# Performance work log

Hardware: AMD Instinct MI355X
Metric: run time of the kernel (lower is better)

The kernel has to match this reference:

```python
import jax, jax.numpy as jnp
import numpy as np

T = 20.0  # temperature
SCALE = 0.3

def reference(outputs1, outputs2, outputs3, outputs4, outputs5, outputs6, outputs7, outputs8, targets):
    # preds: [M=8, B, C] tempered softmaxes
    logits = jnp.stack([outputs1, outputs2, outputs3, outputs4,
                        outputs5, outputs6, outputs7, outputs8], axis=0)
    preds = jax.nn.softmax(logits / T, axis=-1)
    # center over class dim (Pearson correlation per sample per model)
    v = preds - jnp.mean(preds, axis=-1, keepdims=True)
    v = v / jnp.sqrt(jnp.sum(v * v, axis=-1, keepdims=True))  # unit-norm rows
    # Gram over model pairs: [B, M, M]
    G = jnp.einsum('mbc,nbc->bmn', v, v)
    M = G.shape[-1]
    # sum over upper triangle (j<k); diagonal entries are exactly 1 pre-normalization
    d = (jnp.sum(G, axis=(1, 2)) - jnp.trace(G, axis1=1, axis2=2)) * 0.5  # [B]
    loss = SCALE * d
    return jnp.mean(loss)

def setup_inputs() -> dict:
    key = jax.random.key(0)
    ks = jax.random.split(key, 9)
    B, C = 4096, 1000
    inp = {f'outputs{i+1}': jax.random.normal(ks[i], (B, C), dtype=jnp.float32)
           for i in range(8)}
    inp['targets'] = jax.random.randint(ks[8], (B,), 0, C, dtype=jnp.int64)
    return inp
```

## Files before the change

### kernel.cpp

```cpp
#include <hip/hip_runtime.h>
#include <math.h>


constexpr int NC    = 1000;
constexpr int NC4   = 250;
constexpr int NM    = 8;
constexpr int NPAIR = NM * (NM + 1) / 2;
constexpr float KEXP = 0.072134752044448169f;
constexpr float INVC = 1.0f / (float)NC;

__device__ __forceinline__ float waveSum(float v) {
#pragma unroll
    for (int o = 32; o > 0; o >>= 1) v += __shfl_xor(v, o, 64);
    return v;
}
__device__ __forceinline__ double waveSumD(double v) {
#pragma unroll
    for (int o = 32; o > 0; o >>= 1) v += __shfl_xor(v, o, 64);
    return v;
}
__device__ __forceinline__ constexpr int tidx(int m, int n) {
    return m * (2 * NM - m + 1) / 2 + (n - m);
}

__global__ __launch_bounds__(256, 2) void div8_main(
    const float* __restrict__ in0, const float* __restrict__ in1,
    const float* __restrict__ in2, const float* __restrict__ in3,
    const float* __restrict__ in4, const float* __restrict__ in5,
    const float* __restrict__ in6, const float* __restrict__ in7,
    float* __restrict__ part, int B)
{
    const int wid  = threadIdx.x >> 6;
    const int lane = threadIdx.x & 63;
    const int b    = blockIdx.x * 4 + wid;
    if (b >= B) return;
    const bool act3 = lane < (NC4 - 3 * 64);

    const float4* p[NM] = {
        reinterpret_cast<const float4*>(in0 + (size_t)b * NC),
        reinterpret_cast<const float4*>(in1 + (size_t)b * NC),
        reinterpret_cast<const float4*>(in2 + (size_t)b * NC),
        reinterpret_cast<const float4*>(in3 + (size_t)b * NC),
        reinterpret_cast<const float4*>(in4 + (size_t)b * NC),
        reinterpret_cast<const float4*>(in5 + (size_t)b * NC),
        reinterpret_cast<const float4*>(in6 + (size_t)b * NC),
        reinterpret_cast<const float4*>(in7 + (size_t)b * NC) };

    const int   idx[4] = { lane, lane + 64, lane + 128, act3 ? lane + 192 : NC4 - 1 };
    const float msk[4] = { 1.f, 1.f, 1.f, act3 ? 1.f : 0.f };

    float D[NPAIR];
    float t[NM];
#pragma unroll
    for (int k = 0; k < NPAIR; ++k) D[k] = 0.f;
#pragma unroll
    for (int m = 0; m < NM; ++m) t[m] = 0.f;

    float4 cur[NM], nxt[NM];
#pragma unroll
    for (int m = 0; m < NM; ++m) cur[m] = p[m][idx[0]];

#pragma unroll
    for (int j = 0; j < 4; ++j) {
        if (j < 3) {
#pragma unroll
            for (int m = 0; m < NM; ++m) nxt[m] = p[m][idx[j + 1]];
        }
        const float mj = msk[j];
#pragma unroll
        for (int m = 0; m < NM; ++m) {
            cur[m].x = (exp2f(cur[m].x * KEXP) - 1.f) * mj;
            cur[m].y = (exp2f(cur[m].y * KEXP) - 1.f) * mj;
            cur[m].z = (exp2f(cur[m].z * KEXP) - 1.f) * mj;
            cur[m].w = (exp2f(cur[m].w * KEXP) - 1.f) * mj;
        }
#pragma unroll
        for (int comp = 0; comp < 4; ++comp) {
            float us[NM];
#pragma unroll
            for (int m = 0; m < NM; ++m)
                us[m] = (comp == 0) ? cur[m].x : (comp == 1) ? cur[m].y
                      : (comp == 2) ? cur[m].z : cur[m].w;
#pragma unroll
            for (int m = 0; m < NM; ++m) {
                t[m] += us[m];
#pragma unroll
                for (int n = m; n < NM; ++n)
                    D[tidx(m, n)] = fmaf(us[m], us[n], D[tidx(m, n)]);
            }
        }
        if (j < 3) {
#pragma unroll
            for (int m = 0; m < NM; ++m) cur[m] = nxt[m];
        }
    }

#pragma unroll
    for (int k = 0; k < NPAIR; ++k) D[k] = waveSum(D[k]);
#pragma unroll
    for (int m = 0; m < NM; ++m) t[m] = waveSum(t[m]);

    float rm[NM];
#pragma unroll
    for (int m = 0; m < NM; ++m) {
        float q = fmaf(-t[m] * INVC, t[m], D[tidx(m, m)]);
        rm[m] = 1.0f / sqrtf(q);
    }
    double cr = 0.0;
#pragma unroll
    for (int m = 0; m < NM; ++m)
#pragma unroll
        for (int n = m + 1; n < NM; ++n) {
            float cov = fmaf(-t[m] * INVC, t[n], D[tidx(m, n)]);
            cr += (double)(cov * rm[m] * rm[n]);
        }
    if (lane == 0) part[b] = (float)(2.0 * cr);
}

__global__ __launch_bounds__(256) void div8_final(
    const float* __restrict__ part, float* __restrict__ out, int B)
{
    const int t = threadIdx.x;
    double acc = 0.0;
    for (int i = t; i < B; i += 256) acc += (double)part[i];
    acc = waveSumD(acc);
    __shared__ double redd[4];
    if ((t & 63) == 0) redd[t >> 6] = acc;
    __syncthreads();
    if (t == 0) {
        double tot = (redd[0] + redd[1]) + (redd[2] + redd[3]);
        out[0] = (float)(tot * (0.5 * 0.3 / (double)B));
    }
}

extern "C" void kernel_launch(void* const* d_in, const int* in_sizes, int n_in,
                              void* d_out, int out_size, void* d_ws, size_t ws_size,
                              hipStream_t stream)
{
    const float* a0 = (const float*)d_in[0];
    const float* a1 = (const float*)d_in[1];
    const float* a2 = (const float*)d_in[2];
    const float* a3 = (const float*)d_in[3];
    const float* a4 = (const float*)d_in[4];
    const float* a5 = (const float*)d_in[5];
    const float* a6 = (const float*)d_in[6];
    const float* a7 = (const float*)d_in[7];
    const int B = in_sizes[0] / NC;

    float* part = (float*)d_ws;

    const int grid = (B + 3) / 4;
    div8_main<<<grid, 256, 0, stream>>>(a0, a1, a2, a3, a4, a5, a6, a7, part, B);
    div8_final<<<1, 256, 0, stream>>>(part, (float*)d_out, B);
}
```

Before: 38.41 us.

## Split each row across two waves and combine partial Gram sums via LDS

Each sample row is now processed by two wavefronts, each loading two float4 chunks per model up front instead of four with a software-prefetch chain. Partial Gram and sum accumulators are reduced per wave, exchanged through shared memory with a block barrier, and the final correlation is computed from the combined values. The grid doubles and the launch-bounds occupancy hint is dropped. The aim is more memory-level parallelism and shorter per-wave serial work, at the cost of an extra reduction, a barrier and duplicated epilogue math.

```diff
diff --git a/kernel.cpp b/kernel.cpp
--- a/kernel.cpp
+++ b/kernel.cpp
@@ -6,6 +6,7 @@
 constexpr int NC4   = 250;
 constexpr int NM    = 8;
 constexpr int NPAIR = NM * (NM + 1) / 2;
+constexpr int NRED  = NPAIR + NM;
 constexpr float KEXP = 0.072134752044448169f;
 constexpr float INVC = 1.0f / (float)NC;
 
@@ -23,7 +24,7 @@
     return m * (2 * NM - m + 1) / 2 + (n - m);
 }
 
-__global__ __launch_bounds__(256, 2) void div8_main(
+__global__ __launch_bounds__(256) void div8_main(
     const float* __restrict__ in0, const float* __restrict__ in1,
     const float* __restrict__ in2, const float* __restrict__ in3,
     const float* __restrict__ in4, const float* __restrict__ in5,
@@ -32,11 +33,13 @@
 {
     const int wid  = threadIdx.x >> 6;
     const int lane = threadIdx.x & 63;
-    const int b    = blockIdx.x * 4 + wid;
-    if (b >= B) return;
-    const bool act3 = lane < (NC4 - 3 * 64);
+    const int half = wid & 1;
+    const int sloc = wid >> 1;
+    const int braw = blockIdx.x * 2 + sloc;
+    const bool bok = braw < B;
+    const int b    = bok ? braw : (B - 1);
 
-    const float4* p[NM] = {
+    const float4* p4[NM] = {
         reinterpret_cast<const float4*>(in0 + (size_t)b * NC),
         reinterpret_cast<const float4*>(in1 + (size_t)b * NC),
         reinterpret_cast<const float4*>(in2 + (size_t)b * NC),
@@ -46,52 +49,51 @@
         reinterpret_cast<const float4*>(in6 + (size_t)b * NC),
         reinterpret_cast<const float4*>(in7 + (size_t)b * NC) };
 
-    const int   idx[4] = { lane, lane + 64, lane + 128, act3 ? lane + 192 : NC4 - 1 };
-    const float msk[4] = { 1.f, 1.f, 1.f, act3 ? 1.f : 0.f };
+    const bool v1 = (half == 0) || (lane < NC4 - 3 * 64);
+    const int  i0 = half ? (128 + lane) : lane;
+    const int  i1 = half ? (v1 ? 192 + lane : NC4 - 1) : (64 + lane);
+    const float m1 = v1 ? 1.f : 0.f;
 
-    float D[NPAIR];
-    float t[NM];
+    float4 A[NM], Bv[NM];
+#pragma unroll
+    for (int m = 0; m < NM; ++m) A[m]  = p4[m][i0];
+#pragma unroll
+    for (int m = 0; m < NM; ++m) Bv[m] = p4[m][i1];
+
+#pragma unroll
+    for (int m = 0; m < NM; ++m) {
+        A[m].x  = exp2f(A[m].x * KEXP) - 1.f;
+        A[m].y  = exp2f(A[m].y * KEXP) - 1.f;
+        A[m].z  = exp2f(A[m].z * KEXP) - 1.f;
+        A[m].w  = exp2f(A[m].w * KEXP) - 1.f;
+        Bv[m].x = (exp2f(Bv[m].x * KEXP) - 1.f) * m1;
+        Bv[m].y = (exp2f(Bv[m].y * KEXP) - 1.f) * m1;
+        Bv[m].z = (exp2f(Bv[m].z * KEXP) - 1.f) * m1;
+        Bv[m].w = (exp2f(Bv[m].w * KEXP) - 1.f) * m1;
+    }
+
+    float D[NPAIR], t[NM];
 #pragma unroll
     for (int k = 0; k < NPAIR; ++k) D[k] = 0.f;
 #pragma unroll
     for (int m = 0; m < NM; ++m) t[m] = 0.f;
 
-    float4 cur[NM], nxt[NM];
 #pragma unroll
-    for (int m = 0; m < NM; ++m) cur[m] = p[m][idx[0]];
-
-#pragma unroll
-    for (int j = 0; j < 4; ++j) {
-        if (j < 3) {
-#pragma unroll
-            for (int m = 0; m < NM; ++m) nxt[m] = p[m][idx[j + 1]];
-        }
-        const float mj = msk[j];
+    for (int s = 0; s < 8; ++s) {
+        float us[NM];
 #pragma unroll
         for (int m = 0; m < NM; ++m) {
-            cur[m].x = (exp2f(cur[m].x * KEXP) - 1.f) * mj;
-            cur[m].y = (exp2f(cur[m].y * KEXP) - 1.f) * mj;
-            cur[m].z = (exp2f(cur[m].z * KEXP) - 1.f) * mj;
-            cur[m].w = (exp2f(cur[m].w * KEXP) - 1.f) * mj;
+            us[m] = (s == 0) ? A[m].x  : (s == 1) ? A[m].y
+                  : (s == 2) ? A[m].z  : (s == 3) ? A[m].w
+                  : (s == 4) ? Bv[m].x : (s == 5) ? Bv[m].y
+                  : (s == 6) ? Bv[m].z : Bv[m].w;
         }
 #pragma unroll
-        for (int comp = 0; comp < 4; ++comp) {
-            float us[NM];
+        for (int m = 0; m < NM; ++m) {
+            t[m] += us[m];
 #pragma unroll
-            for (int m = 0; m < NM; ++m)
-                us[m] = (comp == 0) ? cur[m].x : (comp == 1) ? cur[m].y
-                      : (comp == 2) ? cur[m].z : cur[m].w;
-#pragma unroll
-            for (int m = 0; m < NM; ++m) {
-                t[m] += us[m];
-#pragma unroll
-                for (int n = m; n < NM; ++n)
-                    D[tidx(m, n)] = fmaf(us[m], us[n], D[tidx(m, n)]);
-            }
-        }
-        if (j < 3) {
-#pragma unroll
-            for (int m = 0; m < NM; ++m) cur[m] = nxt[m];
+            for (int n = m; n < NM; ++n)
+                D[tidx(m, n)] = fmaf(us[m], us[n], D[tidx(m, n)]);
         }
     }
 
@@ -100,10 +102,26 @@
 #pragma unroll
     for (int m = 0; m < NM; ++m) t[m] = waveSum(t[m]);
 
+    __shared__ float comb[2][2][NRED];
+    if (lane == 0) {
+#pragma unroll
+        for (int k = 0; k < NPAIR; ++k) comb[sloc][half][k] = D[k];
+#pragma unroll
+        for (int m = 0; m < NM; ++m) comb[sloc][half][NPAIR + m] = t[m];
+    }
+    __syncthreads();
+
+    float Gd[NPAIR], Gt[NM];
+#pragma unroll
+    for (int k = 0; k < NPAIR; ++k) Gd[k] = comb[sloc][0][k] + comb[sloc][1][k];
+#pragma unroll
+    for (int m = 0; m < NM; ++m)
+        Gt[m] = comb[sloc][0][NPAIR + m] + comb[sloc][1][NPAIR + m];
+
     float rm[NM];
 #pragma unroll
     for (int m = 0; m < NM; ++m) {
-        float q = fmaf(-t[m] * INVC, t[m], D[tidx(m, m)]);
+        float q = fmaf(-Gt[m] * INVC, Gt[m], Gd[tidx(m, m)]);
         rm[m] = 1.0f / sqrtf(q);
     }
     double cr = 0.0;
@@ -111,10 +129,11 @@
     for (int m = 0; m < NM; ++m)
 #pragma unroll
         for (int n = m + 1; n < NM; ++n) {
-            float cov = fmaf(-t[m] * INVC, t[n], D[tidx(m, n)]);
+            float cov = fmaf(-Gt[m] * INVC, Gt[n], Gd[tidx(m, n)]);
             cr += (double)(cov * rm[m] * rm[n]);
         }
-    if (lane == 0) part[b] = (float)(2.0 * cr);
+    if (half == 0 && lane == 0 && bok)
+        part[b] = (float)(2.0 * cr);
 }
 
 __global__ __launch_bounds__(256) void div8_final(
@@ -149,7 +168,7 @@
 
     float* part = (float*)d_ws;
 
-    const int grid = (B + 3) / 4;
+    const int grid = (B + 1) / 2;
     div8_main<<<grid, 256, 0, stream>>>(a0, a1, a2, a3, a4, a5, a6, a7, part, B);
     div8_final<<<1, 256, 0, stream>>>(part, (float*)d_out, B);
 }
```

Result: slower. 45.54 us (+18.6%).
